# Optimization experiments

Hardware: AMD Instinct MI355X
Metric: run time of the kernel (lower is better)

Reference implementation:

```python
import jax, jax.numpy as jnp
import numpy as np

N_USERS = 100000
N_TIRES = 100000
N_BRANDS = 100
N_SIZES = 500
HGT = 128
SPEC = 64
TEXT = 384
TPROJ = 64
HID = 128
OUT = 64
T_EVENTS = 2000000


def _lin_init(key, fan_in, fan_out):
    kw, kb = jax.random.split(key)
    s = 1.0 / np.sqrt(fan_in)
    W = jax.random.uniform(kw, (fan_in, fan_out), jnp.float32, -s, s)
    b = jax.random.uniform(kb, (fan_out,), jnp.float32, -s, s)
    return W, b


def setup_inputs() -> dict:
    key = jax.random.key(0)
    ks = jax.random.split(key, 18)
    inp = {
        "h_user": jax.random.normal(ks[0], (N_USERS, HGT), jnp.float32),
        "h_tire": jax.random.normal(ks[1], (N_TIRES, HGT), jnp.float32),
        "h_brand": jax.random.normal(ks[2], (N_BRANDS, HGT), jnp.float32),
        "h_size": jax.random.normal(ks[3], (N_SIZES, HGT), jnp.float32),
        "tire_specs": jax.random.normal(ks[4], (N_TIRES, SPEC), jnp.float32),
        "text_emb": jax.random.normal(ks[5], (N_TIRES, TEXT), jnp.float32),
        "tire_brand_idx": jax.random.randint(ks[6], (N_TIRES,), 0, N_BRANDS, jnp.int32),
        "tire_size_idx": jax.random.randint(ks[7], (N_TIRES,), 0, N_SIZES, jnp.int32),
        "hist_items": jax.random.randint(ks[8], (T_EVENTS,), 0, N_TIRES, jnp.int32),
        "hist_segments": jnp.sort(jax.random.randint(ks[9], (T_EVENTS,), 0, N_USERS, jnp.int32)),
    }
    # text projection
    inp["W_tp"], inp["b_tp"] = _lin_init(ks[10], TEXT, TPROJ)
    # item tower MLP: in = 3*HGT + SPEC + TPROJ = 512
    item_in = 3 * HGT + SPEC + TPROJ
    inp["W_i1"], inp["b_i1"] = _lin_init(ks[11], item_in, HID)
    inp["W_i2"], inp["b_i2"] = _lin_init(ks[12], HID, HID)
    inp["W_i3"], inp["b_i3"] = _lin_init(ks[13], HID, OUT)
    # user tower MLP: in = HGT + OUT = 192
    user_in = HGT + OUT
    inp["W_u1"], inp["b_u1"] = _lin_init(ks[14], user_in, HID)
    inp["W_u2"], inp["b_u2"] = _lin_init(ks[15], HID, HID)
    inp["W_u3"], inp["b_u3"] = _lin_init(ks[16], HID, OUT)
    return inp


def _mlp(x, W1, b1, W2, b2, W3, b3):
    h = jax.nn.relu(x @ W1 + b1)
    h = jax.nn.relu(h @ W2 + b2)
    return h @ W3 + b3


def _l2norm(x):
    n = jnp.sqrt(jnp.sum(x * x, axis=-1, keepdims=True))
    return x / jnp.maximum(n, 1e-12)


def reference(h_user, h_tire, h_brand, h_size, tire_specs, text_emb,
              tire_brand_idx, tire_size_idx, hist_items, hist_segments,
              W_tp, b_tp, W_i1, b_i1, W_i2, b_i2, W_i3, b_i3,
              W_u1, b_u1, W_u2, b_u2, W_u3, b_u3):
    n_users = h_user.shape[0]
    # item tower (dropout = identity in eval)
    text_proj = jax.nn.relu(text_emb @ W_tp + b_tp)  # [T, 64]
    x_item = jnp.concatenate(
        [h_tire, h_brand[tire_brand_idx], h_size[tire_size_idx], tire_specs, text_proj],
        axis=-1)  # [T, 512]
    item_vec = _l2norm(_mlp(x_item, W_i1, b_i1, W_i2, b_i2, W_i3, b_i3))  # [T, 64]
    # ragged history mean-pool as one segment-mean pass
    gathered = item_vec[hist_items]  # [E, 64]
    sums = jax.ops.segment_sum(gathered, hist_segments, num_segments=n_users)
    counts = jax.ops.segment_sum(jnp.ones((hist_items.shape[0],), item_vec.dtype),
                                 hist_segments, num_segments=n_users)[:, None]
    history_pool = jnp.where(counts > 0, sums / jnp.maximum(counts, 1.0), 0.0)
    # user tower
    x_user = jnp.concatenate([h_user, history_pool], axis=-1)  # [U, 192]
    user_vec = _l2norm(_mlp(x_user, W_u1, b_u1, W_u2, b_u2, W_u3, b_u3))  # [U, 64]
    return user_vec, item_vec
```

## Files before the change

### kernel.cpp

```cpp
#include <hip/hip_runtime.h>

typedef __bf16 bf16;
typedef __bf16 bf16x4 __attribute__((ext_vector_type(4)));
typedef __bf16 bf16x8 __attribute__((ext_vector_type(8)));
typedef float f32x4 __attribute__((ext_vector_type(4)));

__device__ inline float bfbits(unsigned u) { return __builtin_bit_cast(float, u); }

__device__ inline bf16x8 cvt8(const float* p) {
  const f32x4* q = (const f32x4*)p;
  f32x4 x0 = q[0];
  f32x4 x1 = q[1];
  bf16x8 a;
  a[0] = (bf16)x0[0]; a[1] = (bf16)x0[1]; a[2] = (bf16)x0[2]; a[3] = (bf16)x0[3];
  a[4] = (bf16)x1[0]; a[5] = (bf16)x1[1]; a[6] = (bf16)x1[2]; a[7] = (bf16)x1[3];
  return a;
}

struct WEnt { const float* src; bf16* dst; int K; int N; int mode; int base; };
struct WprepArgs { WEnt e[9]; int nent; int total; float* zb; };

__global__ __launch_bounds__(256) void wprep_all(WprepArgs a) {
  int idx = blockIdx.x * 256 + threadIdx.x;
  if (idx < 128) a.zb[idx] = 0.0f;
  if (idx >= a.total) return;
  int ei = 0;
  while (ei + 1 < a.nent && idx >= a.e[ei + 1].base) ++ei;
  const WEnt E = a.e[ei];
  int li = idx - E.base;
  int lane = li & 63, fi = li >> 6;
  int NT = E.N / 16;
  int kt = fi / NT, nt = fi % NT;
  int krow = kt * 32 + ((lane >> 4) << 3);
  int col = nt * 16 + (lane & 15);
  bf16* d = E.dst + (size_t)li * 8;
#pragma unroll
  for (int j = 0; j < 8; ++j) {
    int r = krow + j;
    if (E.mode == 1) r = (r < 128) ? r : r + 256;
    d[j] = (bf16)E.src[(size_t)r * E.N + col];
  }
}

__global__ __launch_bounds__(256) void seg_bounds(const int* __restrict__ hsegs,
                                                  int* __restrict__ bound, int E, int U) {
  int e = blockIdx.x * 256 + threadIdx.x;
  if (e > E) return;
  if (e == 0) {
    int b = hsegs[0];
    for (int u = 0; u <= b; ++u) bound[u] = 0;
  } else if (e == E) {
    int a = hsegs[E - 1];
    for (int u = a + 1; u <= U; ++u) bound[u] = E;
  } else {
    int a = hsegs[e - 1], b = hsegs[e];
    for (int u = a + 1; u <= b; ++u) bound[u] = e;
  }
}

struct GemmArgs {
  const void* a0;
  const bf16* wfrag; const float* bias;
  void* out; void* out2; int M;
};

template <int K, int ASRC>
__device__ inline bf16x8 gemm_load_a(const GemmArgs& g, int r, int kc) {
  if constexpr (ASRC == 0) {
    return cvt8((const float*)g.a0 + (size_t)r * K + kc);
  } else {
    return *(const bf16x8*)((const bf16*)g.a0 + (size_t)r * K + kc);
  }
}

template <int K, int N, int ASRC, int RELU, int OUTM, int NW>
__global__ __launch_bounds__(NW * 64) void gemm_k(GemmArgs g) {
  constexpr int KT = K / 32, NT = N / 16;
  constexpr int TROWS = NW * 32;
  __shared__ bf16 wlds[K * N];
  {
    const uint4* s = (const uint4*)g.wfrag;
    uint4* d = (uint4*)wlds;
    constexpr int CH = K * N * 2 / 16;
    for (int i = threadIdx.x; i < CH; i += NW * 64) d[i] = s[i];
  }
  __syncthreads();

  const int lane = threadIdx.x & 63;
  const int wave = threadIdx.x >> 6;
  const int kgo = (lane >> 4) << 3;
  const int ntiles = (g.M + TROWS - 1) / TROWS;

  for (int tile = blockIdx.x; tile < ntiles; tile += gridDim.x) {
    const int rowbase = tile * TROWS;
    const int rw = rowbase + wave * 16 + (lane & 15);
    const int r0 = min(rw, g.M - 1);
    const int r1 = min(rw + NW * 16, g.M - 1);

    f32x4 acc[2][NT] = {};

#pragma unroll 2
    for (int kt = 0; kt < KT; ++kt) {
      const int kc = kt * 32 + kgo;
      bf16x8 a0 = gemm_load_a<K, ASRC>(g, r0, kc);
      bf16x8 a1 = gemm_load_a<K, ASRC>(g, r1, kc);
      const bf16x8* bp = ((const bf16x8*)wlds) + kt * NT * 64 + lane;
#pragma unroll
      for (int nt = 0; nt < NT; ++nt) {
        bf16x8 b = bp[nt * 64];
        acc[0][nt] = __builtin_amdgcn_mfma_f32_16x16x32_bf16(a0, b, acc[0][nt], 0, 0, 0);
        acc[1][nt] = __builtin_amdgcn_mfma_f32_16x16x32_bf16(a1, b, acc[1][nt], 0, 0, 0);
      }
    }

    const int colbase = lane & 15;
    const int rgrp = (lane >> 4) * 4;
#pragma unroll
    for (int m = 0; m < 2; ++m) {
      const int rbase = rowbase + m * (NW * 16) + wave * 16 + rgrp;
#pragma unroll
      for (int nt = 0; nt < NT; ++nt) {
        const float bv = g.bias[colbase + nt * 16];
        f32x4 dv = acc[m][nt];
#pragma unroll
        for (int j = 0; j < 4; ++j) {
          float v = dv[j] + bv;
          if constexpr (RELU != 0) v = fmaxf(v, 0.0f);
          dv[j] = v;
        }
        acc[m][nt] = dv;
      }
      if constexpr (OUTM == 1) {
#pragma unroll
        for (int j = 0; j < 4; ++j) {
          float ssq = 0.0f;
#pragma unroll
          for (int nt = 0; nt < NT; ++nt) ssq += acc[m][nt][j] * acc[m][nt][j];
          ssq += __shfl_xor(ssq, 1);
          ssq += __shfl_xor(ssq, 2);
          ssq += __shfl_xor(ssq, 4);
          ssq += __shfl_xor(ssq, 8);
          const float scale = 1.0f / fmaxf(sqrtf(ssq), 1e-12f);
          const int r = rbase + j;
          if (r < g.M) {
            float* o = (float*)g.out + (size_t)r * N + colbase;
#pragma unroll
            for (int nt = 0; nt < NT; ++nt) o[nt * 16] = acc[m][nt][j] * scale;
            if (g.out2) {
              bf16* o2 = (bf16*)g.out2 + (size_t)r * N + colbase;
#pragma unroll
              for (int nt = 0; nt < NT; ++nt) o2[nt * 16] = (bf16)(acc[m][nt][j] * scale);
            }
          }
        }
      } else if constexpr (OUTM == 2) {
#pragma unroll
        for (int j = 0; j < 4; ++j) {
          const int r = rbase + j;
          if (r < g.M) {
            float* o = (float*)g.out + (size_t)r * N + colbase;
#pragma unroll
            for (int nt = 0; nt < NT; ++nt) o[nt * 16] = acc[m][nt][j];
          }
        }
      } else {
#pragma unroll
        for (int j = 0; j < 4; ++j) {
          const int r = rbase + j;
          if (r < g.M) {
            bf16* o = (bf16*)g.out + (size_t)r * N + colbase;
#pragma unroll
            for (int nt = 0; nt < NT; ++nt) o[nt * 16] = (bf16)acc[m][nt][j];
          }
        }
      }
    }
  }
}

struct TowerArgs {
  const void* a0; const void* a1; const void* a2;
  const int* bidx; const int* sidx;
  const float* brandC; const float* sizeC;
  const bf16* wf1; const bf16* wf2; const bf16* wf3;
  const float* b1; const float* b2; const float* b3;
  float* out; bf16* out2; int M;
};

template <int ASRC>
__device__ inline bf16x8 tower_load_a(const TowerArgs& g, int r, int kc) {
  if constexpr (ASRC == 2) {
    if (kc < 128) return cvt8((const float*)g.a0 + (size_t)r * 128 + kc);
    else if (kc < 192) return cvt8((const float*)g.a1 + (size_t)r * 64 + (kc - 128));
    else return *(const bf16x8*)((const bf16*)g.a2 + (size_t)r * 64 + (kc - 192));
  } else {
    if (kc < 128) return cvt8((const float*)g.a0 + (size_t)r * 128 + kc);
    else return *(const bf16x8*)((const bf16*)g.a1 + (size_t)r * 64 + (kc - 128));
  }
}

__device__ inline bf16x8 read_afrag(const bf16* hw, int lane, int kt) {
  const int row = lane & 15;
  const int c8 = (kt * 4 + (lane >> 4)) ^ (row & 7);
  return *(const bf16x8*)(hw + row * 128 + c8 * 8);
}

template <int K1, int ASRC, int BS>
__global__ __launch_bounds__(512, 2) void tower_k(TowerArgs g) {
  constexpr int KT1 = K1 / 32;
  constexpr int NW = 8;
  constexpr int TROWS = NW * 32;
  __shared__ bf16 lds[K1 * 128 + 128 * 128 + 128 * 64 + NW * 16 * 128];
  bf16* w1 = lds;
  bf16* w2 = lds + K1 * 128;
  bf16* w3 = w2 + 128 * 128;
  bf16* ht = w3 + 128 * 64;
  {
    const int tid = threadIdx.x;
    const uint4* s1 = (const uint4*)g.wf1; uint4* d1 = (uint4*)w1;
    for (int i = tid; i < K1 * 128 * 2 / 16; i += 512) d1[i] = s1[i];
    const uint4* s2 = (const uint4*)g.wf2; uint4* d2 = (uint4*)w2;
    for (int i = tid; i < 128 * 128 * 2 / 16; i += 512) d2[i] = s2[i];
    const uint4* s3 = (const uint4*)g.wf3; uint4* d3 = (uint4*)w3;
    for (int i = tid; i < 128 * 64 * 2 / 16; i += 512) d3[i] = s3[i];
  }
  __syncthreads();

  const int lane = threadIdx.x & 63;
  const int wave = threadIdx.x >> 6;
  const int kgo = (lane >> 4) << 3;
  const int colbase = lane & 15;
  const int r4 = (lane >> 4) * 4;
  bf16* hw = ht + wave * (16 * 128);
  const int ntiles = (g.M + TROWS - 1) / TROWS;

  for (int tile = blockIdx.x; tile < ntiles; tile += gridDim.x) {
    const int rowbase = tile * TROWS;
    const int rw = rowbase + wave * 16 + colbase;
    const int r0 = min(rw, g.M - 1);
    const int r1 = min(rw + NW * 16, g.M - 1);

    f32x4 acc1[2][8] = {};
#pragma unroll 2
    for (int kt = 0; kt < KT1; ++kt) {
      const int kc = kt * 32 + kgo;
      bf16x8 a0 = tower_load_a<ASRC>(g, r0, kc);
      bf16x8 a1 = tower_load_a<ASRC>(g, r1, kc);
      const bf16x8* bp = ((const bf16x8*)w1) + kt * 8 * 64 + lane;
#pragma unroll
      for (int nt = 0; nt < 8; ++nt) {
        bf16x8 b = bp[nt * 64];
        acc1[0][nt] = __builtin_amdgcn_mfma_f32_16x16x32_bf16(a0, b, acc1[0][nt], 0, 0, 0);
        acc1[1][nt] = __builtin_amdgcn_mfma_f32_16x16x32_bf16(a1, b, acc1[1][nt], 0, 0, 0);
      }
    }

    f32x4 acc3[2][4] = {};
#pragma unroll
    for (int m = 0; m < 2; ++m) {
      const int rbase = rowbase + m * (NW * 16) + wave * 16 + r4;
#pragma unroll
      for (int j = 0; j < 4; ++j) {
        const int row = r4 + j;
        const float* bc = nullptr; const float* sc = nullptr;
        if constexpr (BS != 0) {
          const int rr = min(rbase + j, g.M - 1);
          bc = g.brandC + (size_t)g.bidx[rr] * 128;
          sc = g.sizeC + (size_t)g.sidx[rr] * 128;
        }
#pragma unroll
        for (int nt = 0; nt < 8; ++nt) {
          const int col = colbase + nt * 16;
          float v = acc1[m][nt][j];
          if constexpr (BS != 0) v += bc[col] + sc[col];
          else v += g.b1[col];
          v = fmaxf(v, 0.0f);
          const int c8 = (col >> 3) ^ (row & 7);
          hw[row * 128 + c8 * 8 + (col & 7)] = (bf16)v;
        }
      }
      f32x4 acc2[8] = {};
#pragma unroll
      for (int kt = 0; kt < 4; ++kt) {
        bf16x8 a = read_afrag(hw, lane, kt);
        const bf16x8* bp = ((const bf16x8*)w2) + kt * 8 * 64 + lane;
#pragma unroll
        for (int nt = 0; nt < 8; ++nt)
          acc2[nt] = __builtin_amdgcn_mfma_f32_16x16x32_bf16(a, bp[nt * 64], acc2[nt], 0, 0, 0);
      }
#pragma unroll
      for (int j = 0; j < 4; ++j) {
        const int row = r4 + j;
#pragma unroll
        for (int nt = 0; nt < 8; ++nt) {
          const int col = colbase + nt * 16;
          float v = fmaxf(acc2[nt][j] + g.b2[col], 0.0f);
          const int c8 = (col >> 3) ^ (row & 7);
          hw[row * 128 + c8 * 8 + (col & 7)] = (bf16)v;
        }
      }
#pragma unroll
      for (int kt = 0; kt < 4; ++kt) {
        bf16x8 a = read_afrag(hw, lane, kt);
        const bf16x8* bp = ((const bf16x8*)w3) + kt * 4 * 64 + lane;
#pragma unroll
        for (int nt = 0; nt < 4; ++nt)
          acc3[m][nt] = __builtin_amdgcn_mfma_f32_16x16x32_bf16(a, bp[nt * 64], acc3[m][nt], 0, 0, 0);
      }
    }

#pragma unroll
    for (int m = 0; m < 2; ++m) {
      const int rbase = rowbase + m * (NW * 16) + wave * 16 + r4;
#pragma unroll
      for (int j = 0; j < 4; ++j) {
        float vv[4];
        float ssq = 0.0f;
#pragma unroll
        for (int nt = 0; nt < 4; ++nt) {
          float v = acc3[m][nt][j] + g.b3[colbase + nt * 16];
          vv[nt] = v;
          ssq += v * v;
        }
        ssq += __shfl_xor(ssq, 1);
        ssq += __shfl_xor(ssq, 2);
        ssq += __shfl_xor(ssq, 4);
        ssq += __shfl_xor(ssq, 8);
        const float scale = 1.0f / fmaxf(sqrtf(ssq), 1e-12f);
        const int r = rbase + j;
        if (r < g.M) {
          float* o = g.out + (size_t)r * 64 + colbase;
#pragma unroll
          for (int nt = 0; nt < 4; ++nt) o[nt * 16] = vv[nt] * scale;
          if (g.out2) {
            bf16* o2 = g.out2 + (size_t)r * 64 + colbase;
#pragma unroll
            for (int nt = 0; nt < 4; ++nt) o2[nt * 16] = (bf16)(vv[nt] * scale);
          }
        }
      }
    }
  }
}

__global__ __launch_bounds__(256) void pool_k(const int* __restrict__ hitems,
                                              const int* __restrict__ bound,
                                              const bf16* __restrict__ itemb,
                                              bf16* __restrict__ pool, int U) {
  const int lane = threadIdx.x & 63;
  const int wid = blockIdx.x * 4 + (threadIdx.x >> 6);
  const int stride = gridDim.x * 4;
  const int grp = lane >> 4, li = lane & 15;
  for (int u = wid; u < U; u += stride) {
    const int s = bound[u], e = bound[u + 1];
    f32x4 sa = {0.f, 0.f, 0.f, 0.f}, sb = {0.f, 0.f, 0.f, 0.f};
    int i = s + grp;
    for (; i + 4 < e; i += 8) {
      int it0 = hitems[i];
      int it1 = hitems[i + 4];
      uint2 r0 = *(const uint2*)(itemb + (size_t)it0 * 64 + li * 4);
      uint2 r1 = *(const uint2*)(itemb + (size_t)it1 * 64 + li * 4);
      sa[0] += bfbits(r0.x << 16);      sa[1] += bfbits(r0.x & 0xffff0000u);
      sa[2] += bfbits(r0.y << 16);      sa[3] += bfbits(r0.y & 0xffff0000u);
      sb[0] += bfbits(r1.x << 16);      sb[1] += bfbits(r1.x & 0xffff0000u);
      sb[2] += bfbits(r1.y << 16);      sb[3] += bfbits(r1.y & 0xffff0000u);
    }
    if (i < e) {
      int it0 = hitems[i];
      uint2 r0 = *(const uint2*)(itemb + (size_t)it0 * 64 + li * 4);
      sa[0] += bfbits(r0.x << 16);      sa[1] += bfbits(r0.x & 0xffff0000u);
      sa[2] += bfbits(r0.y << 16);      sa[3] += bfbits(r0.y & 0xffff0000u);
    }
#pragma unroll
    for (int c = 0; c < 4; ++c) sa[c] += sb[c];
#pragma unroll
    for (int c = 0; c < 4; ++c) {
      sa[c] += __shfl_xor(sa[c], 16);
      sa[c] += __shfl_xor(sa[c], 32);
    }
    const int cnt = e - s;
    const float inv = (cnt > 0) ? 1.0f / (float)cnt : 0.0f;
    if (grp == 0) {
      bf16x4 o;
      o[0] = (bf16)(sa[0] * inv); o[1] = (bf16)(sa[1] * inv);
      o[2] = (bf16)(sa[2] * inv); o[3] = (bf16)(sa[3] * inv);
      *(bf16x4*)(pool + (size_t)u * 64 + li * 4) = o;
    }
  }
}

extern "C" void kernel_launch(void* const* d_in, const int* in_sizes, int n_in,
                              void* d_out, int out_size, void* d_ws, size_t ws_size,
                              hipStream_t stream) {
  const float* h_user = (const float*)d_in[0];
  const float* h_tire = (const float*)d_in[1];
  const float* h_brand = (const float*)d_in[2];
  const float* h_size = (const float*)d_in[3];
  const float* specs = (const float*)d_in[4];
  const float* text = (const float*)d_in[5];
  const int* bidx = (const int*)d_in[6];
  const int* sidx = (const int*)d_in[7];
  const int* hitems = (const int*)d_in[8];
  const int* hsegs = (const int*)d_in[9];
  const float* W_tp = (const float*)d_in[10]; const float* b_tp = (const float*)d_in[11];
  const float* W_i1 = (const float*)d_in[12]; const float* b_i1 = (const float*)d_in[13];
  const float* W_i2 = (const float*)d_in[14]; const float* b_i2 = (const float*)d_in[15];
  const float* W_i3 = (const float*)d_in[16]; const float* b_i3 = (const float*)d_in[17];
  const float* W_u1 = (const float*)d_in[18]; const float* b_u1 = (const float*)d_in[19];
  const float* W_u2 = (const float*)d_in[20]; const float* b_u2 = (const float*)d_in[21];
  const float* W_u3 = (const float*)d_in[22]; const float* b_u3 = (const float*)d_in[23];

  const int U = in_sizes[0] / 128;
  const int T = in_sizes[4] / 64;
  const int E = in_sizes[8];

  char* ws = (char*)d_ws;
  size_t off = 0;
  auto alloc = [&](size_t bytes) -> char* {
    char* p = ws + off;
    off += (bytes + 255) & ~(size_t)255;
    return p;
  };
  bf16* wf_tp  = (bf16*)alloc(384 * 64 * 2);
  bf16* wf_i1a = (bf16*)alloc(256 * 128 * 2);
  bf16* wf_ib  = (bf16*)alloc(128 * 128 * 2);
  bf16* wf_is  = (bf16*)alloc(128 * 128 * 2);
  bf16* wf_i2  = (bf16*)alloc(128 * 128 * 2);
  bf16* wf_i3  = (bf16*)alloc(128 * 64 * 2);
  bf16* wf_u1  = (bf16*)alloc(192 * 128 * 2);
  bf16* wf_u2  = (bf16*)alloc(128 * 128 * 2);
  bf16* wf_u3  = (bf16*)alloc(128 * 64 * 2);
  float* zb    = (float*)alloc(128 * 4);
  float* brandC = (float*)alloc(100 * 128 * 4);
  float* sizeC  = (float*)alloc(500 * 128 * 4);
  bf16* tpbuf = (bf16*)alloc((size_t)T * 64 * 2);
  bf16* pool  = (bf16*)alloc((size_t)U * 64 * 2);
  bf16* itemb = (bf16*)alloc((size_t)T * 64 * 2);
  int* bound  = (int*)alloc((size_t)(U + 1) * 4);
  (void)ws_size; (void)n_in; (void)out_size;

  WprepArgs wa = {};
  auto addent = [&](int i, const float* src, bf16* dst, int K, int N, int mode, int& run) {
    wa.e[i] = {src, dst, K, N, mode, run};
    run += (K / 32) * (N / 16) * 64;
  };
  int run = 0;
  addent(0, W_tp, wf_tp, 384, 64, 0, run);
  addent(1, W_i1, wf_i1a, 256, 128, 1, run);
  addent(2, W_i1 + 128 * 128, wf_ib, 128, 128, 0, run);
  addent(3, W_i1 + 256 * 128, wf_is, 128, 128, 0, run);
  addent(4, W_i2, wf_i2, 128, 128, 0, run);
  addent(5, W_i3, wf_i3, 128, 64, 0, run);
  addent(6, W_u1, wf_u1, 192, 128, 0, run);
  addent(7, W_u2, wf_u2, 128, 128, 0, run);
  addent(8, W_u3, wf_u3, 128, 64, 0, run);
  wa.nent = 9; wa.total = run; wa.zb = zb;
  wprep_all<<<(run + 255) / 256, 256, 0, stream>>>(wa);

  seg_bounds<<<(E + 256) / 256, 256, 0, stream>>>(hsegs, bound, E, U);

  {
    GemmArgs a = {}; a.a0 = h_brand; a.wfrag = wf_ib; a.bias = b_i1; a.out = brandC; a.M = 100;
    gemm_k<128, 128, 0, 0, 2, 4><<<1, 256, 0, stream>>>(a);
  }
  {
    GemmArgs a = {}; a.a0 = h_size; a.wfrag = wf_is; a.bias = zb; a.out = sizeC; a.M = 500;
    gemm_k<128, 128, 0, 0, 2, 4><<<4, 256, 0, stream>>>(a);
  }
  {
    GemmArgs a = {}; a.a0 = text; a.wfrag = wf_tp; a.bias = b_tp; a.out = tpbuf; a.M = T;
    gemm_k<384, 64, 0, 1, 0, 4><<<(T + 127) / 128, 256, 0, stream>>>(a);
  }

  float* out_user = (float*)d_out;
  float* out_item = out_user + (size_t)U * 64;

  {
    TowerArgs a = {};
    a.a0 = h_tire; a.a1 = specs; a.a2 = tpbuf;
    a.bidx = bidx; a.sidx = sidx; a.brandC = brandC; a.sizeC = sizeC;
    a.wf1 = wf_i1a; a.wf2 = wf_i2; a.wf3 = wf_i3;
    a.b1 = zb; a.b2 = b_i2; a.b3 = b_i3;
    a.out = out_item; a.out2 = itemb; a.M = T;
    tower_k<256, 2, 1><<<(T + 255) / 256, 512, 0, stream>>>(a);
  }

  pool_k<<<(U + 3) / 4, 256, 0, stream>>>(hitems, bound, itemb, pool, U);

  {
    TowerArgs a = {};
    a.a0 = h_user; a.a1 = pool;
    a.wf1 = wf_u1; a.wf2 = wf_u2; a.wf3 = wf_u3;
    a.b1 = b_u1; a.b2 = b_u2; a.b3 = b_u3;
    a.out = out_user; a.out2 = nullptr; a.M = U;
    tower_k<192, 3, 0><<<(U + 255) / 256, 512, 0, stream>>>(a);
  }
}
```

Measured before the change: 227.1 us.

## Split fused tower kernel into layer-1 and layers-2/3 kernels via bf16 scratch

The fused three-layer tower kernel is split in two. The first kernel computes layer 1 and writes a bf16 hidden buffer to global memory. The second reads that buffer and computes layers 2 and 3, taking W3 fragments straight from global memory instead of LDS. Both kernels have smaller LDS footprints and declare launch bounds of (512,4) instead of (512,2), aiming for higher occupancy. The cost is an extra round trip of a 100k x 128 bf16 buffer through memory, plus an extra launch. The pooling loop is also unrolled to four independent gathers, and unused template paths in gemm_k are removed.

```diff
diff --git a/kernel.cpp b/kernel.cpp
--- a/kernel.cpp
+++ b/kernel.cpp
@@ -61,19 +61,10 @@
 struct GemmArgs {
   const void* a0;
   const bf16* wfrag; const float* bias;
-  void* out; void* out2; int M;
+  void* out; int M;
 };
 
-template <int K, int ASRC>
-__device__ inline bf16x8 gemm_load_a(const GemmArgs& g, int r, int kc) {
-  if constexpr (ASRC == 0) {
-    return cvt8((const float*)g.a0 + (size_t)r * K + kc);
-  } else {
-    return *(const bf16x8*)((const bf16*)g.a0 + (size_t)r * K + kc);
-  }
-}
-
-template <int K, int N, int ASRC, int RELU, int OUTM, int NW>
+template <int K, int N, int RELU, int OUTM, int NW>
 __global__ __launch_bounds__(NW * 64) void gemm_k(GemmArgs g) {
   constexpr int KT = K / 32, NT = N / 16;
   constexpr int TROWS = NW * 32;
@@ -102,8 +93,8 @@
 #pragma unroll 2
     for (int kt = 0; kt < KT; ++kt) {
       const int kc = kt * 32 + kgo;
-      bf16x8 a0 = gemm_load_a<K, ASRC>(g, r0, kc);
-      bf16x8 a1 = gemm_load_a<K, ASRC>(g, r1, kc);
+      bf16x8 a0 = cvt8((const float*)g.a0 + (size_t)r0 * K + kc);
+      bf16x8 a1 = cvt8((const float*)g.a0 + (size_t)r1 * K + kc);
       const bf16x8* bp = ((const bf16x8*)wlds) + kt * NT * 64 + lane;
 #pragma unroll
       for (int nt = 0; nt < NT; ++nt) {
@@ -119,76 +110,35 @@
     for (int m = 0; m < 2; ++m) {
       const int rbase = rowbase + m * (NW * 16) + wave * 16 + rgrp;
 #pragma unroll
-      for (int nt = 0; nt < NT; ++nt) {
-        const float bv = g.bias[colbase + nt * 16];
-        f32x4 dv = acc[m][nt];
-#pragma unroll
-        for (int j = 0; j < 4; ++j) {
-          float v = dv[j] + bv;
-          if constexpr (RELU != 0) v = fmaxf(v, 0.0f);
-          dv[j] = v;
-        }
-        acc[m][nt] = dv;
-      }
-      if constexpr (OUTM == 1) {
-#pragma unroll
-        for (int j = 0; j < 4; ++j) {
-          float ssq = 0.0f;
-#pragma unroll
-          for (int nt = 0; nt < NT; ++nt) ssq += acc[m][nt][j] * acc[m][nt][j];
-          ssq += __shfl_xor(ssq, 1);
-          ssq += __shfl_xor(ssq, 2);
-          ssq += __shfl_xor(ssq, 4);
-          ssq += __shfl_xor(ssq, 8);
-          const float scale = 1.0f / fmaxf(sqrtf(ssq), 1e-12f);
-          const int r = rbase + j;
-          if (r < g.M) {
-            float* o = (float*)g.out + (size_t)r * N + colbase;
-#pragma unroll
-            for (int nt = 0; nt < NT; ++nt) o[nt * 16] = acc[m][nt][j] * scale;
-            if (g.out2) {
-              bf16* o2 = (bf16*)g.out2 + (size_t)r * N + colbase;
-#pragma unroll
-              for (int nt = 0; nt < NT; ++nt) o2[nt * 16] = (bf16)(acc[m][nt][j] * scale);
+      for (int j = 0; j < 4; ++j) {
+        const int r = rbase + j;
+        if (r < g.M) {
+#pragma unroll
+          for (int nt = 0; nt < NT; ++nt) {
+            float v = acc[m][nt][j] + g.bias[colbase + nt * 16];
+            if constexpr (RELU != 0) v = fmaxf(v, 0.0f);
+            if constexpr (OUTM == 2) {
+              ((float*)g.out)[(size_t)r * N + colbase + nt * 16] = v;
+            } else {
+              ((bf16*)g.out)[(size_t)r * N + colbase + nt * 16] = (bf16)v;
             }
           }
         }
-      } else if constexpr (OUTM == 2) {
-#pragma unroll
-        for (int j = 0; j < 4; ++j) {
-          const int r = rbase + j;
-          if (r < g.M) {
-            float* o = (float*)g.out + (size_t)r * N + colbase;
-#pragma unroll
-            for (int nt = 0; nt < NT; ++nt) o[nt * 16] = acc[m][nt][j];
-          }
-        }
-      } else {
-#pragma unroll
-        for (int j = 0; j < 4; ++j) {
-          const int r = rbase + j;
-          if (r < g.M) {
-            bf16* o = (bf16*)g.out + (size_t)r * N + colbase;
-#pragma unroll
-            for (int nt = 0; nt < NT; ++nt) o[nt * 16] = (bf16)acc[m][nt][j];
-          }
-        }
-      }
-    }
-  }
-}
-
-struct TowerArgs {
+      }
+    }
+  }
+}
+
+struct L1Args {
   const void* a0; const void* a1; const void* a2;
   const int* bidx; const int* sidx;
   const float* brandC; const float* sizeC;
-  const bf16* wf1; const bf16* wf2; const bf16* wf3;
-  const float* b1; const float* b2; const float* b3;
-  float* out; bf16* out2; int M;
+  const bf16* wf1; const float* b1;
+  bf16* out; int M;
 };
 
-template <int ASRC>
-__device__ inline bf16x8 tower_load_a(const TowerArgs& g, int r, int kc) {
+template <int K1, int ASRC>
+__device__ inline bf16x8 l1_load_a(const L1Args& g, int r, int kc) {
   if constexpr (ASRC == 2) {
     if (kc < 128) return cvt8((const float*)g.a0 + (size_t)r * 128 + kc);
     else if (kc < 192) return cvt8((const float*)g.a1 + (size_t)r * 64 + (kc - 128));
@@ -199,30 +149,93 @@
   }
 }
 
+template <int K1, int ASRC, int BS>
+__global__ __launch_bounds__(512, 4) void l1_k(L1Args g) {
+  constexpr int KT1 = K1 / 32;
+  constexpr int NW = 8, TROWS = NW * 32;
+  __shared__ bf16 w1[K1 * 128];
+  {
+    const uint4* s = (const uint4*)g.wf1;
+    uint4* d = (uint4*)w1;
+    for (int i = threadIdx.x; i < K1 * 128 * 2 / 16; i += 512) d[i] = s[i];
+  }
+  __syncthreads();
+
+  const int lane = threadIdx.x & 63;
+  const int wave = threadIdx.x >> 6;
+  const int kgo = (lane >> 4) << 3;
+  const int colbase = lane & 15;
+  const int r4 = (lane >> 4) * 4;
+  const int ntiles = (g.M + TROWS - 1) / TROWS;
+
+  for (int tile = blockIdx.x; tile < ntiles; tile += gridDim.x) {
+    const int rowbase = tile * TROWS;
+    const int rw = rowbase + wave * 16 + colbase;
+    const int r0 = min(rw, g.M - 1);
+    const int r1 = min(rw + NW * 16, g.M - 1);
+
+    f32x4 acc1[2][8] = {};
+#pragma unroll 2
+    for (int kt = 0; kt < KT1; ++kt) {
+      const int kc = kt * 32 + kgo;
+      bf16x8 a0 = l1_load_a<K1, ASRC>(g, r0, kc);
+      bf16x8 a1 = l1_load_a<K1, ASRC>(g, r1, kc);
+      const bf16x8* bp = ((const bf16x8*)w1) + kt * 8 * 64 + lane;
+#pragma unroll
+      for (int nt = 0; nt < 8; ++nt) {
+        bf16x8 b = bp[nt * 64];
+        acc1[0][nt] = __builtin_amdgcn_mfma_f32_16x16x32_bf16(a0, b, acc1[0][nt], 0, 0, 0);
+        acc1[1][nt] = __builtin_amdgcn_mfma_f32_16x16x32_bf16(a1, b, acc1[1][nt], 0, 0, 0);
+      }
+    }
+
+#pragma unroll
+    for (int m = 0; m < 2; ++m) {
+      const int rbase = rowbase + m * (NW * 16) + wave * 16 + r4;
+#pragma unroll
+      for (int j = 0; j < 4; ++j) {
+        const int r = rbase + j;
+        const float* bc = nullptr; const float* sc = nullptr;
+        if constexpr (BS != 0) {
+          const int rr = min(r, g.M - 1);
+          bc = g.brandC + (size_t)g.bidx[rr] * 128;
+          sc = g.sizeC + (size_t)g.sidx[rr] * 128;
+        }
+        if (r < g.M) {
+#pragma unroll
+          for (int nt = 0; nt < 8; ++nt) {
+            const int col = colbase + nt * 16;
+            float v = acc1[m][nt][j];
+            if constexpr (BS != 0) v += bc[col] + sc[col];
+            else v += g.b1[col];
+            g.out[(size_t)r * 128 + col] = (bf16)fmaxf(v, 0.0f);
+          }
+        }
+      }
+    }
+  }
+}
+
+struct L23Args {
+  const bf16* h; const bf16* wf2; const bf16* wf3;
+  const float* b2; const float* b3;
+  float* out; bf16* out2; int M;
+};
+
 __device__ inline bf16x8 read_afrag(const bf16* hw, int lane, int kt) {
   const int row = lane & 15;
   const int c8 = (kt * 4 + (lane >> 4)) ^ (row & 7);
   return *(const bf16x8*)(hw + row * 128 + c8 * 8);
 }
 
-template <int K1, int ASRC, int BS>
-__global__ __launch_bounds__(512, 2) void tower_k(TowerArgs g) {
-  constexpr int KT1 = K1 / 32;
-  constexpr int NW = 8;
-  constexpr int TROWS = NW * 32;
-  __shared__ bf16 lds[K1 * 128 + 128 * 128 + 128 * 64 + NW * 16 * 128];
-  bf16* w1 = lds;
-  bf16* w2 = lds + K1 * 128;
-  bf16* w3 = w2 + 128 * 128;
-  bf16* ht = w3 + 128 * 64;
-  {
-    const int tid = threadIdx.x;
-    const uint4* s1 = (const uint4*)g.wf1; uint4* d1 = (uint4*)w1;
-    for (int i = tid; i < K1 * 128 * 2 / 16; i += 512) d1[i] = s1[i];
-    const uint4* s2 = (const uint4*)g.wf2; uint4* d2 = (uint4*)w2;
-    for (int i = tid; i < 128 * 128 * 2 / 16; i += 512) d2[i] = s2[i];
-    const uint4* s3 = (const uint4*)g.wf3; uint4* d3 = (uint4*)w3;
-    for (int i = tid; i < 128 * 64 * 2 / 16; i += 512) d3[i] = s3[i];
+__global__ __launch_bounds__(512, 4) void l23_k(L23Args g) {
+  constexpr int NW = 8, TROWS = NW * 32;
+  __shared__ bf16 w2[128 * 128];
+  __shared__ bf16 ht[NW * 16 * 128];
+  {
+    const uint4* s = (const uint4*)g.wf2;
+    uint4* d = (uint4*)w2;
+    for (int i = threadIdx.x; i < 128 * 128 * 2 / 16; i += 512) d[i] = s[i];
   }
   __syncthreads();
 
@@ -236,57 +249,23 @@
 
   for (int tile = blockIdx.x; tile < ntiles; tile += gridDim.x) {
     const int rowbase = tile * TROWS;
-    const int rw = rowbase + wave * 16 + colbase;
-    const int r0 = min(rw, g.M - 1);
-    const int r1 = min(rw + NW * 16, g.M - 1);
-
-    f32x4 acc1[2][8] = {};
-#pragma unroll 2
-    for (int kt = 0; kt < KT1; ++kt) {
-      const int kc = kt * 32 + kgo;
-      bf16x8 a0 = tower_load_a<ASRC>(g, r0, kc);
-      bf16x8 a1 = tower_load_a<ASRC>(g, r1, kc);
-      const bf16x8* bp = ((const bf16x8*)w1) + kt * 8 * 64 + lane;
-#pragma unroll
-      for (int nt = 0; nt < 8; ++nt) {
-        bf16x8 b = bp[nt * 64];
-        acc1[0][nt] = __builtin_amdgcn_mfma_f32_16x16x32_bf16(a0, b, acc1[0][nt], 0, 0, 0);
-        acc1[1][nt] = __builtin_amdgcn_mfma_f32_16x16x32_bf16(a1, b, acc1[1][nt], 0, 0, 0);
-      }
-    }
-
     f32x4 acc3[2][4] = {};
+
 #pragma unroll
     for (int m = 0; m < 2; ++m) {
-      const int rbase = rowbase + m * (NW * 16) + wave * 16 + r4;
-#pragma unroll
-      for (int j = 0; j < 4; ++j) {
-        const int row = r4 + j;
-        const float* bc = nullptr; const float* sc = nullptr;
-        if constexpr (BS != 0) {
-          const int rr = min(rbase + j, g.M - 1);
-          bc = g.brandC + (size_t)g.bidx[rr] * 128;
-          sc = g.sizeC + (size_t)g.sidx[rr] * 128;
-        }
-#pragma unroll
-        for (int nt = 0; nt < 8; ++nt) {
-          const int col = colbase + nt * 16;
-          float v = acc1[m][nt][j];
-          if constexpr (BS != 0) v += bc[col] + sc[col];
-          else v += g.b1[col];
-          v = fmaxf(v, 0.0f);
-          const int c8 = (col >> 3) ^ (row & 7);
-          hw[row * 128 + c8 * 8 + (col & 7)] = (bf16)v;
-        }
-      }
+      const int rw = rowbase + m * (NW * 16) + wave * 16 + colbase;
+      const int r = min(rw, g.M - 1);
+      bf16x8 a[4];
+#pragma unroll
+      for (int kt = 0; kt < 4; ++kt)
+        a[kt] = *(const bf16x8*)(g.h + (size_t)r * 128 + kt * 32 + kgo);
       f32x4 acc2[8] = {};
 #pragma unroll
       for (int kt = 0; kt < 4; ++kt) {
-        bf16x8 a = read_afrag(hw, lane, kt);
         const bf16x8* bp = ((const bf16x8*)w2) + kt * 8 * 64 + lane;
 #pragma unroll
         for (int nt = 0; nt < 8; ++nt)
-          acc2[nt] = __builtin_amdgcn_mfma_f32_16x16x32_bf16(a, bp[nt * 64], acc2[nt], 0, 0, 0);
+          acc2[nt] = __builtin_amdgcn_mfma_f32_16x16x32_bf16(a[kt], bp[nt * 64], acc2[nt], 0, 0, 0);
       }
 #pragma unroll
       for (int j = 0; j < 4; ++j) {
@@ -301,11 +280,11 @@
       }
 #pragma unroll
       for (int kt = 0; kt < 4; ++kt) {
-        bf16x8 a = read_afrag(hw, lane, kt);
-        const bf16x8* bp = ((const bf16x8*)w3) + kt * 4 * 64 + lane;
+        bf16x8 af = read_afrag(hw, lane, kt);
+        const bf16x8* bp = ((const bf16x8*)g.wf3) + kt * 4 * 64 + lane;
 #pragma unroll
         for (int nt = 0; nt < 4; ++nt)
-          acc3[m][nt] = __builtin_amdgcn_mfma_f32_16x16x32_bf16(a, bp[nt * 64], acc3[m][nt], 0, 0, 0);
+          acc3[m][nt] = __builtin_amdgcn_mfma_f32_16x16x32_bf16(af, bp[nt * 64], acc3[m][nt], 0, 0, 0);
       }
     }
 
@@ -353,37 +332,43 @@
   const int grp = lane >> 4, li = lane & 15;
   for (int u = wid; u < U; u += stride) {
     const int s = bound[u], e = bound[u + 1];
-    f32x4 sa = {0.f, 0.f, 0.f, 0.f}, sb = {0.f, 0.f, 0.f, 0.f};
+    f32x4 s0 = {0.f,0.f,0.f,0.f}, s1 = {0.f,0.f,0.f,0.f};
+    f32x4 s2 = {0.f,0.f,0.f,0.f}, s3 = {0.f,0.f,0.f,0.f};
     int i = s + grp;
-    for (; i + 4 < e; i += 8) {
-      int it0 = hitems[i];
-      int it1 = hitems[i + 4];
-      uint2 r0 = *(const uint2*)(itemb + (size_t)it0 * 64 + li * 4);
-      uint2 r1 = *(const uint2*)(itemb + (size_t)it1 * 64 + li * 4);
-      sa[0] += bfbits(r0.x << 16);      sa[1] += bfbits(r0.x & 0xffff0000u);
-      sa[2] += bfbits(r0.y << 16);      sa[3] += bfbits(r0.y & 0xffff0000u);
-      sb[0] += bfbits(r1.x << 16);      sb[1] += bfbits(r1.x & 0xffff0000u);
-      sb[2] += bfbits(r1.y << 16);      sb[3] += bfbits(r1.y & 0xffff0000u);
-    }
-    if (i < e) {
-      int it0 = hitems[i];
-      uint2 r0 = *(const uint2*)(itemb + (size_t)it0 * 64 + li * 4);
-      sa[0] += bfbits(r0.x << 16);      sa[1] += bfbits(r0.x & 0xffff0000u);
-      sa[2] += bfbits(r0.y << 16);      sa[3] += bfbits(r0.y & 0xffff0000u);
-    }
-#pragma unroll
-    for (int c = 0; c < 4; ++c) sa[c] += sb[c];
+    for (; i + 12 < e; i += 16) {
+      int a0 = hitems[i], a1 = hitems[i + 4], a2 = hitems[i + 8], a3 = hitems[i + 12];
+      uint2 r0 = *(const uint2*)(itemb + (size_t)a0 * 64 + li * 4);
+      uint2 r1 = *(const uint2*)(itemb + (size_t)a1 * 64 + li * 4);
+      uint2 r2 = *(const uint2*)(itemb + (size_t)a2 * 64 + li * 4);
+      uint2 r3 = *(const uint2*)(itemb + (size_t)a3 * 64 + li * 4);
+      s0[0] += bfbits(r0.x << 16); s0[1] += bfbits(r0.x & 0xffff0000u);
+      s0[2] += bfbits(r0.y << 16); s0[3] += bfbits(r0.y & 0xffff0000u);
+      s1[0] += bfbits(r1.x << 16); s1[1] += bfbits(r1.x & 0xffff0000u);
+      s1[2] += bfbits(r1.y << 16); s1[3] += bfbits(r1.y & 0xffff0000u);
+      s2[0] += bfbits(r2.x << 16); s2[1] += bfbits(r2.x & 0xffff0000u);
+      s2[2] += bfbits(r2.y << 16); s2[3] += bfbits(r2.y & 0xffff0000u);
+      s3[0] += bfbits(r3.x << 16); s3[1] += bfbits(r3.x & 0xffff0000u);
+      s3[2] += bfbits(r3.y << 16); s3[3] += bfbits(r3.y & 0xffff0000u);
+    }
+    for (; i < e; i += 4) {
+      int a0 = hitems[i];
+      uint2 r0 = *(const uint2*)(itemb + (size_t)a0 * 64 + li * 4);
+      s0[0] += bfbits(r0.x << 16); s0[1] += bfbits(r0.x & 0xffff0000u);
+      s0[2] += bfbits(r0.y << 16); s0[3] += bfbits(r0.y & 0xffff0000u);
+    }
+#pragma unroll
+    for (int c = 0; c < 4; ++c) s0[c] += s1[c] + s2[c] + s3[c];
 #pragma unroll
     for (int c = 0; c < 4; ++c) {
-      sa[c] += __shfl_xor(sa[c], 16);
-      sa[c] += __shfl_xor(sa[c], 32);
+      s0[c] += __shfl_xor(s0[c], 16);
+      s0[c] += __shfl_xor(s0[c], 32);
     }
     const int cnt = e - s;
     const float inv = (cnt > 0) ? 1.0f / (float)cnt : 0.0f;
     if (grp == 0) {
       bf16x4 o;
-      o[0] = (bf16)(sa[0] * inv); o[1] = (bf16)(sa[1] * inv);
-      o[2] = (bf16)(sa[2] * inv); o[3] = (bf16)(sa[3] * inv);
+      o[0] = (bf16)(s0[0] * inv); o[1] = (bf16)(s0[1] * inv);
+      o[2] = (bf16)(s0[2] * inv); o[3] = (bf16)(s0[3] * inv);
       *(bf16x4*)(pool + (size_t)u * 64 + li * 4) = o;
     }
   }
@@ -434,6 +419,7 @@
   float* brandC = (float*)alloc(100 * 128 * 4);
   float* sizeC  = (float*)alloc(500 * 128 * 4);
   bf16* tpbuf = (bf16*)alloc((size_t)T * 64 * 2);
+  bf16* h1b   = (bf16*)alloc((size_t)T * 128 * 2);
   bf16* pool  = (bf16*)alloc((size_t)U * 64 * 2);
   bf16* itemb = (bf16*)alloc((size_t)T * 64 * 2);
   int* bound  = (int*)alloc((size_t)(U + 1) * 4);
@@ -461,38 +447,47 @@
 
   {
     GemmArgs a = {}; a.a0 = h_brand; a.wfrag = wf_ib; a.bias = b_i1; a.out = brandC; a.M = 100;
-    gemm_k<128, 128, 0, 0, 2, 4><<<1, 256, 0, stream>>>(a);
+    gemm_k<128, 128, 0, 2, 4><<<1, 256, 0, stream>>>(a);
   }
   {
     GemmArgs a = {}; a.a0 = h_size; a.wfrag = wf_is; a.bias = zb; a.out = sizeC; a.M = 500;
-    gemm_k<128, 128, 0, 0, 2, 4><<<4, 256, 0, stream>>>(a);
+    gemm_k<128, 128, 0, 2, 4><<<4, 256, 0, stream>>>(a);
   }
   {
     GemmArgs a = {}; a.a0 = text; a.wfrag = wf_tp; a.bias = b_tp; a.out = tpbuf; a.M = T;
-    gemm_k<384, 64, 0, 1, 0, 4><<<(T + 127) / 128, 256, 0, stream>>>(a);
+    gemm_k<384, 64, 1, 0, 4><<<(T + 127) / 128, 256, 0, stream>>>(a);
   }
 
   float* out_user = (float*)d_out;
   float* out_item = out_user + (size_t)U * 64;
-
-  {
-    TowerArgs a = {};
+  const int tiles256 = (T + 255) / 256;
+
+  {
+    L1Args a = {};
     a.a0 = h_tire; a.a1 = specs; a.a2 = tpbuf;
     a.bidx = bidx; a.sidx = sidx; a.brandC = brandC; a.sizeC = sizeC;
-    a.wf1 = wf_i1a; a.wf2 = wf_i2; a.wf3 = wf_i3;
-    a.b1 = zb; a.b2 = b_i2; a.b3 = b_i3;
+    a.wf1 = wf_i1a; a.b1 = zb; a.out = h1b; a.M = T;
+    l1_k<256, 2, 1><<<tiles256, 512, 0, stream>>>(a);
+  }
+  {
+    L23Args a = {};
+    a.h = h1b; a.wf2 = wf_i2; a.wf3 = wf_i3; a.b2 = b_i2; a.b3 = b_i3;
     a.out = out_item; a.out2 = itemb; a.M = T;
-    tower_k<256, 2, 1><<<(T + 255) / 256, 512, 0, stream>>>(a);
+    l23_k<<<tiles256, 512, 0, stream>>>(a);
   }
 
   pool_k<<<(U + 3) / 4, 256, 0, stream>>>(hitems, bound, itemb, pool, U);
 
   {
-    TowerArgs a = {};
+    L1Args a = {};
     a.a0 = h_user; a.a1 = pool;
-    a.wf1 = wf_u1; a.wf2 = wf_u2; a.wf3 = wf_u3;
-    a.b1 = b_u1; a.b2 = b_u2; a.b3 = b_u3;
+    a.wf1 = wf_u1; a.b1 = b_u1; a.out = h1b; a.M = U;
+    l1_k<192, 3, 0><<<(U + 255) / 256, 512, 0, stream>>>(a);
+  }
+  {
+    L23Args a = {};
+    a.h = h1b; a.wf2 = wf_u2; a.wf3 = wf_u3; a.b2 = b_u2; a.b3 = b_u3;
     a.out = out_user; a.out2 = nullptr; a.M = U;
-    tower_k<192, 3, 0><<<(U + 255) / 256, 512, 0, stream>>>(a);
-  }
-}
+    l23_k<<<(U + 255) / 256, 512, 0, stream>>>(a);
+  }
+}
```

New measurement: 292.2 us. +28.7%, slower.
